# Performance work log

Hardware: AMD Instinct MI355X
Metric: run time of the kernel (lower is better)

The kernel has to match this reference:

```python
import jax, jax.numpy as jnp
import numpy as np

B, H, W, C = 2, 64, 64, 1024
L = H * W
HC, WC = 32, 32
NH, DH = 16, 64
NUM_REMAIN = 1638


def setup_inputs() -> dict:
    key = jax.random.key(0)
    ks = jax.random.split(key, 8)
    s = 1.0 / np.sqrt(C)
    x = jax.random.normal(ks[0], (B, L, C), jnp.float32)
    cached_x = jax.random.normal(ks[1], (B, HC, WC, C), jnp.float32)
    W_qkv = jax.random.normal(ks[2], (3 * C, C), jnp.float32) * s
    q_bias = jnp.zeros((C,), jnp.float32)
    v_bias = jnp.zeros((C,), jnp.float32)
    W_proj = jax.random.normal(ks[3], (C, C), jnp.float32) * s
    b_proj = jnp.zeros((C,), jnp.float32)
    scale_mul_log = jnp.full((1, NH, 1, 1), np.log(4.0), jnp.float32)
    # rope cache as (cos, sin) pairs over the flat token axis, DH//2 freqs
    ang = jax.random.uniform(ks[4], (L, DH // 2), jnp.float32) * (2 * np.pi)
    rope_grid = jnp.stack([jnp.cos(ang), jnp.sin(ang)], axis=0)  # (2, L, DH//2)
    return {"x": x, "cached_x": cached_x, "W_qkv": W_qkv, "q_bias": q_bias,
            "v_bias": v_bias, "W_proj": W_proj, "b_proj": b_proj,
            "scale_mul_log": scale_mul_log, "rope_grid": rope_grid,
            "num_remain": NUM_REMAIN}


def reference(x, cached_x, W_qkv, q_bias, v_bias, W_proj, b_proj,
              scale_mul_log, rope_grid, num_remain):
    Bx, Lx, Cx = x.shape
    # --- FastVAR token merge: MSE-to-spatial-mean selection (adaptive_avg_pool2d -> mean over L)
    mean_x = jnp.mean(x, axis=1, keepdims=True)                      # (B,1,C)
    mse = jnp.sum((x - mean_x) ** 2, axis=-1)                        # (B,L)
    idx = jnp.argsort(-mse, axis=1)[:, :num_remain]                  # (B,n) descending
    bix = jnp.arange(Bx)[:, None]
    xm = x[bix, idx]                                                 # (B,n,C) merged tokens
    # --- qkv projection with (q_bias, 0, v_bias)
    bias = jnp.concatenate([q_bias, jnp.zeros_like(q_bias), v_bias])
    qkv = (xm @ W_qkv.T + bias).reshape(Bx, -1, 3, NH, DH)
    qkv = qkv.transpose(2, 0, 3, 1, 4)                               # (3,B,H,n,dh)
    q, k, v = qkv[0], qkv[1], qkv[2]
    # --- cos attention: L2-normalize q,k; head-wise learned scale on q; sdpa scale = 1
    scale_mul = jnp.exp(jnp.minimum(scale_mul_log, jnp.log(100.0)))  # (1,NH,1,1)
    def l2n(t):
        return t / jnp.maximum(jnp.linalg.norm(t, axis=-1, keepdims=True), 1e-12)
    q = l2n(q) * scale_mul
    k = l2n(k)
    # --- 2D RoPE with per-sample gathered cache at the kept-token positions
    rc = rope_grid[:, idx, :]                                        # (2,B,n,DH//2)
    r0 = rc[0][:, None, :, :]                                        # (B,1,n,DH//2)
    r1 = rc[1][:, None, :, :]
    def rope(t):
        tp = t.reshape(*t.shape[:-1], DH // 2, 2)
        t0, t1 = tp[..., 0], tp[..., 1]
        return jnp.stack([r0 * t0 - r1 * t1, r1 * t0 + r0 * t1], axis=-1).reshape(t.shape)
    q = rope(q)
    k = rope(k)
    # --- attention over merged tokens
    attn = jax.nn.softmax(jnp.einsum('bhqd,bhkd->bhqk', q, k), axis=-1)
    o = jnp.einsum('bhqk,bhkd->bhqd', attn, v)                       # (B,H,n,dh)
    o = o.transpose(0, 2, 1, 3).reshape(Bx, -1, Cx)                  # (B,n,C)
    o = o @ W_proj.T + b_proj
    up = jnp.repeat(jnp.repeat(cached_x, 2, axis=1), 2, axis=2).reshape(Bx, Lx, Cx)
    out_full = up.at[bix, idx].set(o)
    return x + out_full
```

## Files before the change

### kernel.cpp

```cpp
#include <hip/hip_runtime.h>
#include <hip/hip_bf16.h>
#include <math.h>

#define BQ   2
#define LQ   4096
#define CQ   1024
#define NHQ  16
#define DHQ  64
#define KSEL 1638
#define KPAD 1664
#define MTOT (BQ*KSEL)
#define MPAD 3328

typedef short s16x8 __attribute__((ext_vector_type(8)));
typedef float fx4   __attribute__((ext_vector_type(4)));

#define MFMA16(a,b,c) __builtin_amdgcn_mfma_f32_16x16x32_bf16(a,b,c,0,0,0)

__device__ __forceinline__ float b2f(unsigned short u) {
  union { float f; unsigned int i; } cv; cv.i = ((unsigned int)u) << 16; return cv.f;
}
__device__ __forceinline__ unsigned short f2b(float f) {
  union { float f; unsigned int i; } cv; cv.f = f;
  unsigned int x = cv.i;
  return (unsigned short)((x + 0x7fffu + ((x >> 16) & 1u)) >> 16);
}
__device__ __forceinline__ unsigned int fbits(float f) {
  union { float f; unsigned int i; } cv; cv.f = f; return cv.i;
}
__device__ __forceinline__ unsigned int cvtpk_bf16(float a, float b) {
  unsigned int r;
  asm("v_cvt_pk_bf16_f32 %0, %1, %2" : "=v"(r) : "v"(a), "v"(b));
  return r;
}
__device__ __forceinline__ void async16(const void* g, void* l) {
  __builtin_amdgcn_global_load_lds((const __attribute__((address_space(1))) void*)g,
                                   (__attribute__((address_space(3))) void*)l, 16, 0, 0);
}
__device__ __forceinline__ float fexp2(float x) {
#if __has_builtin(__builtin_amdgcn_exp2f)
  return __builtin_amdgcn_exp2f(x);
#else
  return __expf(x * 0.69314718055994531f);
#endif
}

__global__ __launch_bounds__(256) void k_mean_part(const float* __restrict__ x,
                                                   double* __restrict__ part) {
  int bid = blockIdx.x;
  int cb = bid & 3, ch = (bid >> 2) & 31, b = bid >> 7;
  int c = cb * 256 + threadIdx.x;
  const float* p = x + ((size_t)b * LQ + (size_t)ch * 128) * CQ + c;
  double s = 0.0;
  for (int r = 0; r < 128; ++r) s += (double)p[(size_t)r * CQ];
  part[((size_t)b * 32 + ch) * CQ + c] = s;
}

__global__ __launch_bounds__(256) void k_mean_reduce(const double* __restrict__ part,
                                                     double* __restrict__ mean) {
  int g = blockIdx.x * 256 + threadIdx.x;
  int b = g >> 10, c = g & 1023;
  double s = 0.0;
  for (int ch = 0; ch < 32; ++ch) s += part[((size_t)b * 32 + ch) * CQ + c];
  mean[g] = s * (1.0 / 4096.0);
}

__global__ __launch_bounds__(256) void k_mse_base(const float* __restrict__ x,
                                                  const float* __restrict__ cached,
                                                  const double* __restrict__ mean,
                                                  double* __restrict__ mse,
                                                  float* __restrict__ out,
                                                  unsigned short* __restrict__ xb) {
  int bl = blockIdx.x; int b = bl >> 12, l = bl & 4095;
  int hh = l >> 6, ww = l & 63;
  size_t xoff = ((size_t)b * LQ + l) * CQ;
  size_t uoff = (((size_t)b * 32 + (hh >> 1)) * 32 + (ww >> 1)) * CQ;
  const double* mrow = mean + (size_t)b * CQ;
  int c0 = threadIdx.x * 4;
  float4 xv = *(const float4*)(x + xoff + c0);
  float4 uv = *(const float4*)(cached + uoff + c0);
  float4 ov;
  ov.x = xv.x + uv.x; ov.y = xv.y + uv.y; ov.z = xv.z + uv.z; ov.w = xv.w + uv.w;
  *(float4*)(out + xoff + c0) = ov;
  ushort4 xo;
  xo.x = f2b(xv.x); xo.y = f2b(xv.y); xo.z = f2b(xv.z); xo.w = f2b(xv.w);
  ((ushort4*)xb)[(xoff + c0) >> 2] = xo;
  double d0 = (double)xv.x - mrow[c0];
  double d1 = (double)xv.y - mrow[c0 + 1];
  double d2 = (double)xv.z - mrow[c0 + 2];
  double d3 = (double)xv.w - mrow[c0 + 3];
  double ss = d0 * d0 + d1 * d1 + d2 * d2 + d3 * d3;
  for (int o = 1; o < 64; o <<= 1) ss += __shfl_xor(ss, o);
  __shared__ double ws4[4];
  if ((threadIdx.x & 63) == 0) ws4[threadIdx.x >> 6] = ss;
  __syncthreads();
  if (threadIdx.x == 0) mse[(size_t)b * LQ + l] = ws4[0] + ws4[1] + ws4[2] + ws4[3];
}

__global__ __launch_bounds__(1024) void k_topk(const double* __restrict__ mse,
                                               int* __restrict__ idx_sel,
                                               const float* __restrict__ wqkv,
                                               const float* __restrict__ wproj,
                                               unsigned short* __restrict__ wqb,
                                               unsigned short* __restrict__ wpb) {
  if (blockIdx.x >= 2) {
    int i = (blockIdx.x - 2) * 1024 + threadIdx.x;
    const float* s; unsigned short* d; int off;
    if (i < 786432) { s = wqkv;  d = wqb; off = i; }
    else            { s = wproj; d = wpb; off = i - 786432; }
    float4 v = ((const float4*)s)[off];
    ushort4 o;
    o.x = f2b(v.x); o.y = f2b(v.y); o.z = f2b(v.z); o.w = f2b(v.w);
    ((ushort4*)d)[off] = o;
    return;
  }
  __shared__ unsigned long long u[4096];
  __shared__ unsigned int whist[16 * 257];
  __shared__ unsigned int wtot[4];
  __shared__ unsigned long long sh_prefix;
  __shared__ int sh_rem, sh_rem2, sh_bsel, sh_cnt, sh_eqcnt;
  __shared__ int eqbuf[256];
  int b = blockIdx.x, t = threadIdx.x;
  int wv = t >> 6, laneid = t & 63;
  for (int p = 0; p < 4; ++p) {
    int i = p * 1024 + t;
    u[i] = (unsigned long long)__double_as_longlong(mse[(size_t)b * LQ + i]);
  }
  if (t == 0) { sh_prefix = 0ULL; sh_rem = KSEL; sh_cnt = 0; sh_eqcnt = 0; }
  __syncthreads();
  for (int shift = 56; shift >= 0; shift -= 8) {
    for (int z = t; z < 16 * 257; z += 1024) whist[z] = 0u;
    __syncthreads();
    unsigned long long pref = sh_prefix;
#pragma unroll
    for (int p = 0; p < 4; ++p) {
      int i = p * 1024 + t;
      unsigned long long v = u[i];
      bool cand = (shift == 56) || ((v >> ((shift + 8) & 63)) == pref);
      if (cand) atomicAdd(&whist[wv * 257 + ((unsigned int)(v >> shift) & 255u)], 1u);
    }
    __syncthreads();
    unsigned int myc = 0, mysc = 0;
    if (t < 256) {
      unsigned int s = 0;
      int bin = 255 - t;
#pragma unroll
      for (int wvi = 0; wvi < 16; ++wvi) s += whist[wvi * 257 + bin];
      myc = s;
      mysc = myc;
#pragma unroll
      for (int o = 1; o < 64; o <<= 1) {
        unsigned int v2 = __shfl_up(mysc, o);
        if (laneid >= o) mysc += v2;
      }
      if (laneid == 63) wtot[wv] = mysc;
    }
    __syncthreads();
    if (t < 256) {
      unsigned int basep = 0;
      for (int wvi = 0; wvi < wv; ++wvi) basep += wtot[wvi];
      unsigned int incl = basep + mysc;
      unsigned int excl = incl - myc;
      unsigned int rem = (unsigned int)sh_rem;
      if (excl < rem && rem <= incl) {
        sh_bsel = 255 - t;
        sh_rem2 = (int)(rem - excl);
      }
    }
    __syncthreads();
    if (t == 0) {
      sh_prefix = (sh_prefix << 8) | (unsigned long long)sh_bsel;
      sh_rem = sh_rem2;
    }
    __syncthreads();
  }
  unsigned long long T = sh_prefix;
  int rem_eq = sh_rem;
#pragma unroll
  for (int p = 0; p < 4; ++p) {
    int i = p * 1024 + t;
    unsigned long long v = u[i];
    bool win = (v > T);
    unsigned long long mask = __ballot(win);
    int total = __popcll(mask);
    int base = 0;
    if (laneid == 0 && total > 0) base = atomicAdd(&sh_cnt, total);
    base = __shfl(base, 0);
    if (win) {
      int lpos = __popcll(mask & ((1ULL << laneid) - 1ULL));
      idx_sel[b * KPAD + base + lpos] = i;
    }
    if (v == T) {
      int e = atomicAdd(&sh_eqcnt, 1);
      if (e < 256) eqbuf[e] = i;
    }
  }
  __syncthreads();
  if (t == 0) {
    int n = sh_eqcnt; if (n > 256) n = 256;
    for (int a = 1; a < n; ++a) {
      int key = eqbuf[a]; int c = a - 1;
      while (c >= 0 && eqbuf[c] > key) { eqbuf[c + 1] = eqbuf[c]; --c; }
      eqbuf[c + 1] = key;
    }
    int base = sh_cnt;
    for (int a = 0; a < rem_eq && a < n; ++a) idx_sel[b * KPAD + base + a] = eqbuf[a];
    for (int a = KSEL; a < KPAD; ++a) idx_sel[b * KPAD + a] = 0;
  }
}

__global__ __launch_bounds__(256) void k_gemmA(const unsigned short* __restrict__ Asrc,
                                               const unsigned short* __restrict__ Bmat,
                                               const int* __restrict__ idx_sel,
                                               unsigned short* __restrict__ Cbf) {
  int bm = blockIdx.x % 26, bn = blockIdx.x / 26;
  int tid = threadIdx.x;
  int w = tid >> 6, lane = tid & 63, quad = lane >> 4, l15 = lane & 15;
  int wm = w & 1, wn = w >> 1;
  __shared__ __align__(16) unsigned char sm[3][16384];

  const unsigned short* gA[2];
  const unsigned short* gB[2];
#pragma unroll
  for (int p = 0; p < 2; ++p) {
    int e = p * 256 + tid; int row = e >> 2, kc = e & 3;
    int m = bm * 128 + row; if (m >= MTOT) m = MTOT - 1;
    int bb = m / KSEL; int ii = m - bb * KSEL;
    int lsel = idx_sel[bb * KPAD + ii];
    gA[p] = Asrc + ((size_t)bb * LQ + lsel) * CQ + kc * 8;
    gB[p] = Bmat + (size_t)(bn * 128 + row) * CQ + kc * 8;
  }

  fx4 acc[4][4];
#pragma unroll
  for (int a = 0; a < 4; ++a)
#pragma unroll
    for (int c = 0; c < 4; ++c) acc[a][c] = (fx4){0.f, 0.f, 0.f, 0.f};

#define STAGE_A(boff, it) do { int ke = (it) * 32;                                  \
    _Pragma("unroll")                                                               \
    for (int p = 0; p < 2; ++p) {                                                   \
      async16(gA[p] + ke, sm[0] + (boff) + p * 4096 + w * 1024);                    \
      async16(gB[p] + ke, sm[0] + (boff) + 8192 + p * 4096 + w * 1024);             \
    } } while (0)

  STAGE_A(0, 0);
  STAGE_A(16384, 1);
  for (int it = 0; it < 32; ++it) {
    int cur = it % 3;
    if (it + 2 < 32) STAGE_A(((it + 2) % 3) * 16384, it + 2);
    if (it <= 29)      asm volatile("s_waitcnt vmcnt(8)");
    else if (it == 30) asm volatile("s_waitcnt vmcnt(4)");
    else               asm volatile("s_waitcnt vmcnt(0)");
    __builtin_amdgcn_s_barrier();
    const unsigned char* smb = sm[0] + cur * 16384;
    s16x8 af[4], bf[4];
#pragma unroll
    for (int mt = 0; mt < 4; ++mt)
      af[mt] = *(const s16x8*)(smb + ((wm * 64 + mt * 16 + l15) * 64 + quad * 16));
#pragma unroll
    for (int nt = 0; nt < 4; ++nt)
      bf[nt] = *(const s16x8*)(smb + 8192 + ((wn * 64 + nt * 16 + l15) * 64 + quad * 16));
    __builtin_amdgcn_s_setprio(1);
#pragma unroll
    for (int mt = 0; mt < 4; ++mt)
#pragma unroll
      for (int nt = 0; nt < 4; ++nt)
        acc[mt][nt] = MFMA16(af[mt], bf[nt], acc[mt][nt]);
    __builtin_amdgcn_s_setprio(0);
    __builtin_amdgcn_s_barrier();
  }
#undef STAGE_A

#pragma unroll
  for (int mt = 0; mt < 4; ++mt)
#pragma unroll
    for (int nt = 0; nt < 4; ++nt) {
      int n = bn * 128 + wn * 64 + nt * 16 + l15;
      int mbase = bm * 128 + wm * 64 + mt * 16 + quad * 4;
      fx4 vv = acc[mt][nt];
#pragma unroll
      for (int r = 0; r < 4; ++r) {
        int m = mbase + r;
        if (m < MTOT) Cbf[(size_t)m * 3072 + n] = f2b(vv[r]);
      }
    }
}

__global__ __launch_bounds__(256) void k_gemmB(const unsigned short* __restrict__ Asrc,
                                               const unsigned short* __restrict__ Bmat,
                                               const int* __restrict__ idx_sel,
                                               float* __restrict__ Cf,
                                               const float* __restrict__ xin,
                                               const float* __restrict__ bproj) {
  int bid = blockIdx.x;
  int swz = (bid & 7) * 104 + (bid >> 3);
  int bm = swz % 52, bn = swz / 52;
  int tid = threadIdx.x;
  int w = tid >> 6, lane = tid & 63, quad = lane >> 4, l15 = lane & 15;
  int wm = w & 1, wn = w >> 1;
  __shared__ __align__(16) unsigned char sm[2][16384];

  const unsigned short* g4[4];
#pragma unroll
  for (int p = 0; p < 4; ++p) {
    int e = (p & 1) * 256 + tid; int row = e >> 3, kc = e & 7;
    if (p < 2) {
      int m = bm * 64 + row; if (m >= MTOT) m = MTOT - 1;
      int bb = m / KSEL; int ii = m - bb * KSEL;
      g4[p] = Asrc + ((size_t)bb * KPAD + ii) * CQ + kc * 8;
    } else {
      g4[p] = Bmat + (size_t)(bn * 64 + row) * CQ + kc * 8;
    }
  }

  fx4 acc[2][2];
#pragma unroll
  for (int a = 0; a < 2; ++a)
#pragma unroll
    for (int c = 0; c < 2; ++c) acc[a][c] = (fx4){0.f, 0.f, 0.f, 0.f};

#define STAGE_B(buf, it) do { int ke = (it) * 64;                                   \
    _Pragma("unroll")                                                               \
    for (int p = 0; p < 4; ++p)                                                     \
      async16(g4[p] + ke, sm[buf] + p * 4096 + w * 1024);                           \
    } while (0)

  STAGE_B(0, 0);
  for (int it = 0; it < 16; ++it) {
    int cur = it & 1;
    if (it < 15) STAGE_B(cur ^ 1, it + 1);
    if (it < 15) asm volatile("s_waitcnt vmcnt(4)");
    else         asm volatile("s_waitcnt vmcnt(0)");
    __builtin_amdgcn_s_barrier();
    const unsigned char* smb = sm[cur];
#pragma unroll
    for (int kk = 0; kk < 2; ++kk) {
      s16x8 af[2], bf2[2];
#pragma unroll
      for (int mt = 0; mt < 2; ++mt)
        af[mt] = *(const s16x8*)(smb + ((wm * 32 + mt * 16 + l15) * 64 + kk * 32 + quad * 8) * 2);
#pragma unroll
      for (int nt = 0; nt < 2; ++nt)
        bf2[nt] = *(const s16x8*)(smb + 8192 + ((wn * 32 + nt * 16 + l15) * 64 + kk * 32 + quad * 8) * 2);
#pragma unroll
      for (int mt = 0; mt < 2; ++mt)
#pragma unroll
        for (int nt = 0; nt < 2; ++nt)
          acc[mt][nt] = MFMA16(af[mt], bf2[nt], acc[mt][nt]);
    }
    __builtin_amdgcn_s_barrier();
  }
#undef STAGE_B

#pragma unroll
  for (int mt = 0; mt < 2; ++mt)
#pragma unroll
    for (int nt = 0; nt < 2; ++nt) {
      int n = bn * 64 + wn * 32 + nt * 16 + l15;
      int mbase = bm * 64 + wm * 32 + mt * 16 + quad * 4;
      fx4 vv = acc[mt][nt];
      float bp = bproj[n];
#pragma unroll
      for (int r = 0; r < 4; ++r) {
        int m = mbase + r;
        if (m < MTOT) {
          int bb = m / KSEL; int ii = m - bb * KSEL;
          int lsel = idx_sel[bb * KPAD + ii];
          size_t off = ((size_t)bb * LQ + lsel) * CQ + n;
          Cf[off] = xin[off] + vv[r] + bp;
        }
      }
    }
}

__global__ __launch_bounds__(256) void k_normrope(const unsigned short* __restrict__ qkv,
                                                  const int* __restrict__ idx_sel,
                                                  const float* __restrict__ qbias,
                                                  const float* __restrict__ vbias,
                                                  const float* __restrict__ sml,
                                                  const float* __restrict__ rope,
                                                  unsigned short* __restrict__ qo,
                                                  unsigned short* __restrict__ ko,
                                                  unsigned short* __restrict__ vt) {
  int bid = blockIdx.x;
  int tile = bid % 26; int h = (bid / 26) & 15; int b = bid / (26 * 16);
  int tid = threadIdx.x; int w = tid >> 6; int d = tid & 63;
  __shared__ unsigned short vtile[64 * 68];
  float scale = expf(fminf(sml[h], 4.6051702f)) * 1.4426950408889634f;
  float qb = qbias[h * 64 + d];
  float vb = vbias[h * 64 + d];
  for (int pass = 0; pass < 16; ++pass) {
    int il = pass * 4 + w;
    int i = tile * 64 + il;
    float vraw = 0.f;
    if (i < KSEL) {
      int lsel = idx_sel[b * KPAD + i];
      size_t base = ((size_t)(b * KSEL + i)) * 3072 + h * 64 + d;
      int tt = d >> 1;
      float r0 = rope[(size_t)lsel * 32 + tt];
      float r1 = rope[(size_t)LQ * 32 + (size_t)lsel * 32 + tt];
      float qv = b2f(qkv[base]) + qb;
      float ss = qv * qv;
      for (int o = 1; o < 64; o <<= 1) ss += __shfl_xor(ss, o);
      float qn = qv / fmaxf(sqrtf(ss), 1e-12f) * scale;
      float qp = __shfl_xor(qn, 1);
      float qr = (d & 1) ? (r1 * qp + r0 * qn) : (r0 * qn - r1 * qp);
      qo[((size_t)(b * NHQ + h) * KPAD + i) * 64 + d] = f2b(qr);
      float kv = b2f(qkv[base + 1024]);
      float ks = kv * kv;
      for (int o = 1; o < 64; o <<= 1) ks += __shfl_xor(ks, o);
      float kn = kv / fmaxf(sqrtf(ks), 1e-12f);
      float kp = __shfl_xor(kn, 1);
      float kr = (d & 1) ? (r1 * kp + r0 * kn) : (r0 * kn - r1 * kp);
      ko[((size_t)(b * NHQ + h) * KPAD + i) * 64 + d] = f2b(kr);
      vraw = b2f(qkv[base + 2048]) + vb;
    }
    vtile[d * 68 + il] = f2b(vraw);
  }
  __syncthreads();
  int row = tid >> 2, c0 = (tid & 3) * 16;
  s16x8 o0, o1;
#pragma unroll
  for (int jj = 0; jj < 8; ++jj) {
    o0[jj] = (short)vtile[row * 68 + c0 + jj];
    o1[jj] = (short)vtile[row * 68 + c0 + 8 + jj];
  }
  size_t doff = ((size_t)((b * NHQ + h) * 64 + row)) * KPAD + (size_t)tile * 64 + c0;
  *(s16x8*)(vt + doff) = o0;
  *(s16x8*)(vt + doff + 8) = o1;
}

__global__ __launch_bounds__(256, 4) void k_attn(const unsigned short* __restrict__ qb,
                                                 const unsigned short* __restrict__ kb,
                                                 const unsigned short* __restrict__ vtb,
                                                 const float* __restrict__ sml,
                                                 unsigned short* __restrict__ pO,
                                                 float* __restrict__ pl) {
  int qt = blockIdx.x; int bh = blockIdx.y; int part = blockIdx.z;
  int b = bh >> 4, h = bh & 15;
  int t0 = part * 13, t1 = t0 + 13;
  int q0 = qt * 128;
  int tid = threadIdx.x, w = tid >> 6, lane = tid & 63, quad = lane >> 4, l15 = lane & 15;
  float M = __expf(fminf(sml[h], 4.6051702f)) * 1.4426950408889634f;
  __shared__ __align__(16) unsigned short Kt[64 * 72];
  __shared__ __align__(16) unsigned short Vt[64 * 72];
  __shared__ __align__(16) unsigned short Pq[4][32 * 72];
  unsigned short* Pw = Pq[w];
  const unsigned short* qbase = qb + (size_t)(b * NHQ + h) * KPAD * 64;
  const unsigned short* kbase = kb + (size_t)(b * NHQ + h) * KPAD * 64;
  const unsigned short* vbase = vtb + (size_t)(b * NHQ + h) * 64 * KPAD;

  int r0 = tid >> 3, c0 = tid & 7;
  int r1 = 32 + r0, c1 = c0;

  s16x8 qf[2][2];
#pragma unroll
  for (int qtile = 0; qtile < 2; ++qtile)
#pragma unroll
    for (int kb2 = 0; kb2 < 2; ++kb2) {
      int row = q0 + w * 32 + qtile * 16 + l15;
      qf[qtile][kb2] = *(const s16x8*)(qbase + (size_t)row * 64 + kb2 * 32 + quad * 8);
    }

  float lsum[2] = {0.f, 0.f};
  fx4 oacc[2][4];
#pragma unroll
  for (int qtile = 0; qtile < 2; ++qtile)
#pragma unroll
    for (int dt = 0; dt < 4; ++dt) oacc[qtile][dt] = (fx4){0.f, 0.f, 0.f, 0.f};

  s16x8 kn0, kn1, vn0, vn1;
  {
    int j0 = t0 * 64;
    kn0 = *(const s16x8*)(kbase + (size_t)(j0 + r0) * 64 + c0 * 8);
    kn1 = *(const s16x8*)(kbase + (size_t)(j0 + r1) * 64 + c1 * 8);
    vn0 = *(const s16x8*)(vbase + (size_t)r0 * KPAD + j0 + c0 * 8);
    vn1 = *(const s16x8*)(vbase + (size_t)r1 * KPAD + j0 + c1 * 8);
  }

  for (int t = t0; t < t1; ++t) {
    int j0 = t * 64;
    bool tail = (j0 + 64 > KSEL);
    __builtin_amdgcn_s_barrier();
    *(s16x8*)(Kt + r0 * 72 + c0 * 8) = kn0;
    *(s16x8*)(Kt + r1 * 72 + c1 * 8) = kn1;
    *(s16x8*)(Vt + r0 * 72 + c0 * 8) = vn0;
    *(s16x8*)(Vt + r1 * 72 + c1 * 8) = vn1;
    if (t + 1 < t1) {
      int jn = (t + 1) * 64;
      kn0 = *(const s16x8*)(kbase + (size_t)(jn + r0) * 64 + c0 * 8);
      kn1 = *(const s16x8*)(kbase + (size_t)(jn + r1) * 64 + c1 * 8);
      vn0 = *(const s16x8*)(vbase + (size_t)r0 * KPAD + jn + c0 * 8);
      vn1 = *(const s16x8*)(vbase + (size_t)r1 * KPAD + jn + c1 * 8);
    }
    asm volatile("s_waitcnt lgkmcnt(0)" ::: "memory");
    __builtin_amdgcn_s_barrier();

    fx4 sacc[2][4];
#pragma unroll
    for (int qtile = 0; qtile < 2; ++qtile)
#pragma unroll
      for (int jj = 0; jj < 4; ++jj) sacc[qtile][jj] = (fx4){0.f, 0.f, 0.f, 0.f};
    __builtin_amdgcn_s_setprio(1);
#pragma unroll
    for (int jj = 0; jj < 4; ++jj) {
      int jl = jj * 16 + l15;
      s16x8 kf0 = *(const s16x8*)(Kt + jl * 72 + quad * 8);
      s16x8 kf1 = *(const s16x8*)(Kt + jl * 72 + 32 + quad * 8);
      sacc[0][jj] = MFMA16(kf0, qf[0][0], sacc[0][jj]);
      sacc[1][jj] = MFMA16(kf0, qf[1][0], sacc[1][jj]);
      sacc[0][jj] = MFMA16(kf1, qf[0][1], sacc[0][jj]);
      sacc[1][jj] = MFMA16(kf1, qf[1][1], sacc[1][jj]);
    }
    __builtin_amdgcn_s_setprio(0);
#pragma unroll
    for (int qtile = 0; qtile < 2; ++qtile)
#pragma unroll
      for (int jj = 0; jj < 4; ++jj) {
        int jbase = j0 + jj * 16 + quad * 4;
        fx4 sv = sacc[qtile][jj];
        float p0 = fexp2(sv[0] - M);
        float p1 = fexp2(sv[1] - M);
        float p2 = fexp2(sv[2] - M);
        float p3 = fexp2(sv[3] - M);
        if (tail) {
          if (jbase + 0 >= KSEL) p0 = 0.f;
          if (jbase + 1 >= KSEL) p1 = 0.f;
          if (jbase + 2 >= KSEL) p2 = 0.f;
          if (jbase + 3 >= KSEL) p3 = 0.f;
        }
        lsum[qtile] += (p0 + p1) + (p2 + p3);
        *(uint2*)(Pw + (qtile * 16 + l15) * 72 + jj * 16 + quad * 4) =
            make_uint2(cvtpk_bf16(p0, p1), cvtpk_bf16(p2, p3));
      }
    __builtin_amdgcn_s_setprio(1);
#pragma unroll
    for (int js = 0; js < 2; ++js) {
      s16x8 pf0 = *(const s16x8*)(Pw + l15 * 72 + js * 32 + quad * 8);
      s16x8 pf1 = *(const s16x8*)(Pw + (16 + l15) * 72 + js * 32 + quad * 8);
#pragma unroll
      for (int dt = 0; dt < 4; ++dt) {
        s16x8 vf = *(const s16x8*)(Vt + (dt * 16 + l15) * 72 + js * 32 + quad * 8);
        oacc[0][dt] = MFMA16(pf0, vf, oacc[0][dt]);
        oacc[1][dt] = MFMA16(pf1, vf, oacc[1][dt]);
      }
    }
    __builtin_amdgcn_s_setprio(0);
  }

#pragma unroll
  for (int qtile = 0; qtile < 2; ++qtile) {
    float s = lsum[qtile];
    s += __shfl_xor(s, 16);
    s += __shfl_xor(s, 32);
    lsum[qtile] = s;
  }

  size_t pbase = (((size_t)part * 2 + b) * NHQ + h) * KPAD;
#pragma unroll
  for (int qtile = 0; qtile < 2; ++qtile) {
    int gqb = q0 + w * 32 + qtile * 16;
    if (quad == 0) pl[pbase + gqb + l15] = lsum[qtile];
  }

#pragma unroll
  for (int qtile = 0; qtile < 2; ++qtile)
#pragma unroll
    for (int dt = 0; dt < 4; ++dt)
#pragma unroll
      for (int r = 0; r < 4; ++r)
        Pw[(qtile * 16 + quad * 4 + r) * 72 + dt * 16 + l15] = f2b(oacc[qtile][dt][r]);
#pragma unroll
  for (int pass = 0; pass < 4; ++pass) {
    int row = pass * 8 + (lane >> 3), chunk = lane & 7;
    s16x8 vv = *(const s16x8*)(Pw + row * 72 + chunk * 8);
    *(s16x8*)(pO + (pbase + q0 + w * 32 + row) * 64 + chunk * 8) = vv;
  }
}

__global__ __launch_bounds__(256) void k_comb(const unsigned short* __restrict__ pO,
                                              const float* __restrict__ pl,
                                              unsigned short* __restrict__ ob) {
  size_t g = (size_t)blockIdx.x * 256 + threadIdx.x;
  int d = (int)(g & 63);
  size_t row = g >> 6;
  int gq = (int)(row % KPAD);
  int bhh = (int)(row / KPAD);
  int b = bhh >> 4, h = bhh & 15;
  float oa = b2f(pO[g]);
  float obv = b2f(pO[g + 3407872]);
  float la = pl[row], lb = pl[row + 53248];
  float o = (oa + obv) / (la + lb);
  ob[((size_t)(b * KPAD + gq)) * CQ + h * 64 + d] = f2b(o);
}

extern "C" void kernel_launch(void* const* d_in, const int* in_sizes, int n_in,
                              void* d_out, int out_size, void* d_ws, size_t ws_size,
                              hipStream_t stream) {
  const float* x      = (const float*)d_in[0];
  const float* cached = (const float*)d_in[1];
  const float* wqkv   = (const float*)d_in[2];
  const float* qbias  = (const float*)d_in[3];
  const float* vbias  = (const float*)d_in[4];
  const float* wproj  = (const float*)d_in[5];
  const float* bproj  = (const float*)d_in[6];
  const float* sml    = (const float*)d_in[7];
  const float* rope   = (const float*)d_in[8];
  float* out = (float*)d_out;
  char* ws = (char*)d_ws;

  double* meanpart        = (double*)(ws);
  double* mean            = (double*)(ws + 524288);
  double* mse             = (double*)(ws + 540672);
  int* idx_sel            = (int*)(ws + 606208);
  unsigned short* x_bf    = (unsigned short*)(ws + 619520);
  unsigned short* wqkv_bf = (unsigned short*)(ws + 17396736);
  unsigned short* qkv     = (unsigned short*)(ws + 23688192);
  unsigned short* pO      = (unsigned short*)(ws + 619520);
  float* pl               = (float*)(ws + 14251008);
  unsigned short* wproj_bf= (unsigned short*)(ws + 44135424);
  unsigned short* qo      = (unsigned short*)(ws + 46232576);
  unsigned short* ko      = (unsigned short*)(ws + 53048320);
  unsigned short* vt      = (unsigned short*)(ws + 59864064);
  unsigned short* ob      = (unsigned short*)(ws + 66679808);

  hipLaunchKernelGGL(k_mean_part, dim3(256), dim3(256), 0, stream, x, meanpart);
  hipLaunchKernelGGL(k_mean_reduce, dim3(8), dim3(256), 0, stream, meanpart, mean);
  hipLaunchKernelGGL(k_mse_base, dim3(8192), dim3(256), 0, stream, x, cached, mean, mse,
                     out, x_bf);
  hipLaunchKernelGGL(k_topk, dim3(2 + 1024), dim3(1024), 0, stream, mse, idx_sel,
                     wqkv, wproj, wqkv_bf, wproj_bf);
  hipLaunchKernelGGL(k_gemmA, dim3(26 * 24), dim3(256), 0, stream,
                     x_bf, wqkv_bf, idx_sel, qkv);
  hipLaunchKernelGGL(k_normrope, dim3(26 * 16 * BQ), dim3(256), 0, stream,
                     qkv, idx_sel, qbias, vbias, sml, rope, qo, ko, vt);
  hipLaunchKernelGGL(k_attn, dim3(13, BQ * NHQ, 2), dim3(256), 0, stream,
                     qo, ko, vt, sml, pO, pl);
  hipLaunchKernelGGL(k_comb, dim3(13312), dim3(256), 0, stream, pO, pl, ob);
  hipLaunchKernelGGL(k_gemmB, dim3(832), dim3(256), 0, stream,
                     ob, wproj_bf, idx_sel, out, x, bproj);
}
```

Before: 282.7 us.

## Split attention KV range four ways and shrink P buffer for occupancy

Attention now splits the key range into four partitions (7,7,6,6 tiles) instead of two, doubling the block count. To raise occupancy (launch bounds 8), the per-warp P staging buffer is halved: softmax and the PV MFMAs are interleaved per 32-key half, and the output epilogue is written in two halves. The combine kernel sums four partials and the partial-sum buffer is moved to make room. The cost is more partial-output traffic and a heavier combine step.

```diff
diff --git a/kernel.cpp b/kernel.cpp
--- a/kernel.cpp
+++ b/kernel.cpp
@@ -431,7 +431,7 @@
   *(s16x8*)(vt + doff + 8) = o1;
 }
 
-__global__ __launch_bounds__(256, 4) void k_attn(const unsigned short* __restrict__ qb,
+__global__ __launch_bounds__(256, 8) void k_attn(const unsigned short* __restrict__ qb,
                                                  const unsigned short* __restrict__ kb,
                                                  const unsigned short* __restrict__ vtb,
                                                  const float* __restrict__ sml,
@@ -439,13 +439,15 @@
                                                  float* __restrict__ pl) {
   int qt = blockIdx.x; int bh = blockIdx.y; int part = blockIdx.z;
   int b = bh >> 4, h = bh & 15;
-  int t0 = part * 13, t1 = t0 + 13;
+  int t0, t1;
+  if (part < 2) { t0 = part * 7; t1 = t0 + 7; }
+  else          { t0 = 14 + (part - 2) * 6; t1 = t0 + 6; }
   int q0 = qt * 128;
   int tid = threadIdx.x, w = tid >> 6, lane = tid & 63, quad = lane >> 4, l15 = lane & 15;
   float M = __expf(fminf(sml[h], 4.6051702f)) * 1.4426950408889634f;
   __shared__ __align__(16) unsigned short Kt[64 * 72];
   __shared__ __align__(16) unsigned short Vt[64 * 72];
-  __shared__ __align__(16) unsigned short Pq[4][32 * 72];
+  __shared__ __align__(16) unsigned short Pq[4][32 * 40];
   unsigned short* Pw = Pq[w];
   const unsigned short* qbase = qb + (size_t)(b * NHQ + h) * KPAD * 64;
   const unsigned short* kbase = kb + (size_t)(b * NHQ + h) * KPAD * 64;
@@ -514,39 +516,43 @@
       sacc[1][jj] = MFMA16(kf1, qf[1][1], sacc[1][jj]);
     }
     __builtin_amdgcn_s_setprio(0);
-#pragma unroll
-    for (int qtile = 0; qtile < 2; ++qtile)
-#pragma unroll
-      for (int jj = 0; jj < 4; ++jj) {
-        int jbase = j0 + jj * 16 + quad * 4;
-        fx4 sv = sacc[qtile][jj];
-        float p0 = fexp2(sv[0] - M);
-        float p1 = fexp2(sv[1] - M);
-        float p2 = fexp2(sv[2] - M);
-        float p3 = fexp2(sv[3] - M);
-        if (tail) {
-          if (jbase + 0 >= KSEL) p0 = 0.f;
-          if (jbase + 1 >= KSEL) p1 = 0.f;
-          if (jbase + 2 >= KSEL) p2 = 0.f;
-          if (jbase + 3 >= KSEL) p3 = 0.f;
+
+#pragma unroll
+    for (int js = 0; js < 2; ++js) {
+#pragma unroll
+      for (int qtile = 0; qtile < 2; ++qtile)
+#pragma unroll
+        for (int jg = 0; jg < 2; ++jg) {
+          int jj = js * 2 + jg;
+          int jbase = j0 + jj * 16 + quad * 4;
+          fx4 sv = sacc[qtile][jj];
+          float p0 = fexp2(sv[0] - M);
+          float p1 = fexp2(sv[1] - M);
+          float p2 = fexp2(sv[2] - M);
+          float p3 = fexp2(sv[3] - M);
+          if (tail) {
+            if (jbase + 0 >= KSEL) p0 = 0.f;
+            if (jbase + 1 >= KSEL) p1 = 0.f;
+            if (jbase + 2 >= KSEL) p2 = 0.f;
+            if (jbase + 3 >= KSEL) p3 = 0.f;
+          }
+          lsum[qtile] += (p0 + p1) + (p2 + p3);
+          *(uint2*)(Pw + (qtile * 16 + l15) * 40 + jg * 16 + quad * 4) =
+              make_uint2(cvtpk_bf16(p0, p1), cvtpk_bf16(p2, p3));
         }
-        lsum[qtile] += (p0 + p1) + (p2 + p3);
-        *(uint2*)(Pw + (qtile * 16 + l15) * 72 + jj * 16 + quad * 4) =
-            make_uint2(cvtpk_bf16(p0, p1), cvtpk_bf16(p2, p3));
+      __builtin_amdgcn_s_setprio(1);
+      {
+        s16x8 pf0 = *(const s16x8*)(Pw + l15 * 40 + quad * 8);
+        s16x8 pf1 = *(const s16x8*)(Pw + (16 + l15) * 40 + quad * 8);
+#pragma unroll
+        for (int dt = 0; dt < 4; ++dt) {
+          s16x8 vf = *(const s16x8*)(Vt + (dt * 16 + l15) * 72 + js * 32 + quad * 8);
+          oacc[0][dt] = MFMA16(pf0, vf, oacc[0][dt]);
+          oacc[1][dt] = MFMA16(pf1, vf, oacc[1][dt]);
+        }
       }
-    __builtin_amdgcn_s_setprio(1);
-#pragma unroll
-    for (int js = 0; js < 2; ++js) {
-      s16x8 pf0 = *(const s16x8*)(Pw + l15 * 72 + js * 32 + quad * 8);
-      s16x8 pf1 = *(const s16x8*)(Pw + (16 + l15) * 72 + js * 32 + quad * 8);
-#pragma unroll
-      for (int dt = 0; dt < 4; ++dt) {
-        s16x8 vf = *(const s16x8*)(Vt + (dt * 16 + l15) * 72 + js * 32 + quad * 8);
-        oacc[0][dt] = MFMA16(pf0, vf, oacc[0][dt]);
-        oacc[1][dt] = MFMA16(pf1, vf, oacc[1][dt]);
-      }
-    }
-    __builtin_amdgcn_s_setprio(0);
+      __builtin_amdgcn_s_setprio(0);
+    }
   }
 
 #pragma unroll
@@ -565,17 +571,23 @@
   }
 
 #pragma unroll
-  for (int qtile = 0; qtile < 2; ++qtile)
-#pragma unroll
-    for (int dt = 0; dt < 4; ++dt)
-#pragma unroll
-      for (int r = 0; r < 4; ++r)
-        Pw[(qtile * 16 + quad * 4 + r) * 72 + dt * 16 + l15] = f2b(oacc[qtile][dt][r]);
-#pragma unroll
-  for (int pass = 0; pass < 4; ++pass) {
-    int row = pass * 8 + (lane >> 3), chunk = lane & 7;
-    s16x8 vv = *(const s16x8*)(Pw + row * 72 + chunk * 8);
-    *(s16x8*)(pO + (pbase + q0 + w * 32 + row) * 64 + chunk * 8) = vv;
+  for (int half = 0; half < 2; ++half) {
+    __builtin_amdgcn_s_barrier();
+#pragma unroll
+    for (int qtile = 0; qtile < 2; ++qtile)
+#pragma unroll
+      for (int dt = 0; dt < 2; ++dt)
+#pragma unroll
+        for (int r = 0; r < 4; ++r)
+          Pw[(qtile * 16 + quad * 4 + r) * 40 + dt * 16 + l15] =
+              f2b(oacc[qtile][half * 2 + dt][r]);
+    asm volatile("s_waitcnt lgkmcnt(0)" ::: "memory");
+#pragma unroll
+    for (int pass = 0; pass < 2; ++pass) {
+      int row = pass * 16 + (lane >> 2), chunk = lane & 3;
+      s16x8 vv = *(const s16x8*)(Pw + row * 40 + chunk * 8);
+      *(s16x8*)(pO + (pbase + q0 + w * 32 + row) * 64 + half * 32 + chunk * 8) = vv;
+    }
   }
 }
 
@@ -588,10 +600,13 @@
   int gq = (int)(row % KPAD);
   int bhh = (int)(row / KPAD);
   int b = bhh >> 4, h = bhh & 15;
-  float oa = b2f(pO[g]);
-  float obv = b2f(pO[g + 3407872]);
-  float la = pl[row], lb = pl[row + 53248];
-  float o = (oa + obv) / (la + lb);
+  float osum = 0.f, lsumv = 0.f;
+#pragma unroll
+  for (int p = 0; p < 4; ++p) {
+    osum += b2f(pO[g + (size_t)p * 3407872]);
+    lsumv += pl[row + (size_t)p * 53248];
+  }
+  float o = osum / lsumv;
   ob[((size_t)(b * KPAD + gq)) * CQ + h * 64 + d] = f2b(o);
 }
 
@@ -618,7 +633,7 @@
   unsigned short* wqkv_bf = (unsigned short*)(ws + 17396736);
   unsigned short* qkv     = (unsigned short*)(ws + 23688192);
   unsigned short* pO      = (unsigned short*)(ws + 619520);
-  float* pl               = (float*)(ws + 14251008);
+  float* pl               = (float*)(ws + 27882496);
   unsigned short* wproj_bf= (unsigned short*)(ws + 44135424);
   unsigned short* qo      = (unsigned short*)(ws + 46232576);
   unsigned short* ko      = (unsigned short*)(ws + 53048320);
@@ -635,7 +650,7 @@
                      x_bf, wqkv_bf, idx_sel, qkv);
   hipLaunchKernelGGL(k_normrope, dim3(26 * 16 * BQ), dim3(256), 0, stream,
                      qkv, idx_sel, qbias, vbias, sml, rope, qo, ko, vt);
-  hipLaunchKernelGGL(k_attn, dim3(13, BQ * NHQ, 2), dim3(256), 0, stream,
+  hipLaunchKernelGGL(k_attn, dim3(13, BQ * NHQ, 4), dim3(256), 0, stream,
                      qo, ko, vt, sml, pO, pl);
   hipLaunchKernelGGL(k_comb, dim3(13312), dim3(256), 0, stream, pO, pl, ob);
   hipLaunchKernelGGL(k_gemmB, dim3(832), dim3(256), 0, stream,
```

New measurement: 290.4 us. 2.7% more time.

## Shrink QKV GEMM tile to 64x128 with double buffering; vectorize norm-rope

Applied to the files above, without the earlier changes.

The QKV projection GEMM now uses 64-row M tiles instead of 128 and a two-stage LDS buffer instead of three. That doubles the grid to 1248 blocks so more CUs have work, and it reduces LDS and accumulator use per block. The cost is less data reuse per tile and a shallower prefetch pipeline. Separately, the norm+RoPE kernel now has each lane handle a pair of dims with 32-bit loads and stores, two tokens per wave, and shorter shuffle reductions.

```diff
diff --git a/kernel.cpp b/kernel.cpp
--- a/kernel.cpp
+++ b/kernel.cpp
@@ -213,57 +213,56 @@
                                                const unsigned short* __restrict__ Bmat,
                                                const int* __restrict__ idx_sel,
                                                unsigned short* __restrict__ Cbf) {
-  int bm = blockIdx.x % 26, bn = blockIdx.x / 26;
+  int bm = blockIdx.x % 52, bn = blockIdx.x / 52;
   int tid = threadIdx.x;
   int w = tid >> 6, lane = tid & 63, quad = lane >> 4, l15 = lane & 15;
   int wm = w & 1, wn = w >> 1;
-  __shared__ __align__(16) unsigned char sm[3][16384];
-
-  const unsigned short* gA[2];
+  __shared__ __align__(16) unsigned char sm[2][12288];
+
+  const unsigned short* gA;
+  {
+    int row = tid >> 2, kc = tid & 3;
+    int m = bm * 64 + row; if (m >= MTOT) m = MTOT - 1;
+    int bb = m / KSEL; int ii = m - bb * KSEL;
+    int lsel = idx_sel[bb * KPAD + ii];
+    gA = Asrc + ((size_t)bb * LQ + lsel) * CQ + kc * 8;
+  }
   const unsigned short* gB[2];
 #pragma unroll
   for (int p = 0; p < 2; ++p) {
     int e = p * 256 + tid; int row = e >> 2, kc = e & 3;
-    int m = bm * 128 + row; if (m >= MTOT) m = MTOT - 1;
-    int bb = m / KSEL; int ii = m - bb * KSEL;
-    int lsel = idx_sel[bb * KPAD + ii];
-    gA[p] = Asrc + ((size_t)bb * LQ + lsel) * CQ + kc * 8;
     gB[p] = Bmat + (size_t)(bn * 128 + row) * CQ + kc * 8;
   }
 
-  fx4 acc[4][4];
-#pragma unroll
-  for (int a = 0; a < 4; ++a)
+  fx4 acc[2][4];
+#pragma unroll
+  for (int a = 0; a < 2; ++a)
 #pragma unroll
     for (int c = 0; c < 4; ++c) acc[a][c] = (fx4){0.f, 0.f, 0.f, 0.f};
 
-#define STAGE_A(boff, it) do { int ke = (it) * 32;                                  \
-    _Pragma("unroll")                                                               \
-    for (int p = 0; p < 2; ++p) {                                                   \
-      async16(gA[p] + ke, sm[0] + (boff) + p * 4096 + w * 1024);                    \
-      async16(gB[p] + ke, sm[0] + (boff) + 8192 + p * 4096 + w * 1024);             \
-    } } while (0)
+#define STAGE_A(buf, it) do { int ke = (it) * 32;                                   \
+    async16(gA + ke, sm[buf] + tid * 16);                                           \
+    async16(gB[0] + ke, sm[buf] + 4096 + tid * 16);                                 \
+    async16(gB[1] + ke, sm[buf] + 8192 + tid * 16); } while (0)
 
   STAGE_A(0, 0);
-  STAGE_A(16384, 1);
   for (int it = 0; it < 32; ++it) {
-    int cur = it % 3;
-    if (it + 2 < 32) STAGE_A(((it + 2) % 3) * 16384, it + 2);
-    if (it <= 29)      asm volatile("s_waitcnt vmcnt(8)");
-    else if (it == 30) asm volatile("s_waitcnt vmcnt(4)");
-    else               asm volatile("s_waitcnt vmcnt(0)");
+    int cur = it & 1;
+    if (it < 31) STAGE_A(cur ^ 1, it + 1);
+    if (it < 31) asm volatile("s_waitcnt vmcnt(3)");
+    else         asm volatile("s_waitcnt vmcnt(0)");
     __builtin_amdgcn_s_barrier();
-    const unsigned char* smb = sm[0] + cur * 16384;
-    s16x8 af[4], bf[4];
-#pragma unroll
-    for (int mt = 0; mt < 4; ++mt)
-      af[mt] = *(const s16x8*)(smb + ((wm * 64 + mt * 16 + l15) * 64 + quad * 16));
+    const unsigned char* smb = sm[cur];
+    s16x8 af[2], bf[4];
+#pragma unroll
+    for (int mt = 0; mt < 2; ++mt)
+      af[mt] = *(const s16x8*)(smb + ((wm * 32 + mt * 16 + l15) * 32 + quad * 8) * 2);
 #pragma unroll
     for (int nt = 0; nt < 4; ++nt)
-      bf[nt] = *(const s16x8*)(smb + 8192 + ((wn * 64 + nt * 16 + l15) * 64 + quad * 16));
+      bf[nt] = *(const s16x8*)(smb + 4096 + ((wn * 64 + nt * 16 + l15) * 32 + quad * 8) * 2);
     __builtin_amdgcn_s_setprio(1);
 #pragma unroll
-    for (int mt = 0; mt < 4; ++mt)
+    for (int mt = 0; mt < 2; ++mt)
 #pragma unroll
       for (int nt = 0; nt < 4; ++nt)
         acc[mt][nt] = MFMA16(af[mt], bf[nt], acc[mt][nt]);
@@ -273,11 +272,11 @@
 #undef STAGE_A
 
 #pragma unroll
-  for (int mt = 0; mt < 4; ++mt)
+  for (int mt = 0; mt < 2; ++mt)
 #pragma unroll
     for (int nt = 0; nt < 4; ++nt) {
       int n = bn * 128 + wn * 64 + nt * 16 + l15;
-      int mbase = bm * 128 + wm * 64 + mt * 16 + quad * 4;
+      int mbase = bm * 64 + wm * 32 + mt * 16 + quad * 4;
       fx4 vv = acc[mt][nt];
 #pragma unroll
       for (int r = 0; r < 4; ++r) {
@@ -385,38 +384,48 @@
                                                   unsigned short* __restrict__ vt) {
   int bid = blockIdx.x;
   int tile = bid % 26; int h = (bid / 26) & 15; int b = bid / (26 * 16);
-  int tid = threadIdx.x; int w = tid >> 6; int d = tid & 63;
+  int tid = threadIdx.x; int w = tid >> 6; int lane = tid & 63;
+  int tk = lane >> 5, dl = lane & 31;
+  int d0 = dl * 2;
   __shared__ unsigned short vtile[64 * 68];
   float scale = expf(fminf(sml[h], 4.6051702f)) * 1.4426950408889634f;
-  float qb = qbias[h * 64 + d];
-  float vb = vbias[h * 64 + d];
-  for (int pass = 0; pass < 16; ++pass) {
-    int il = pass * 4 + w;
+  float2 qb2 = *(const float2*)(qbias + h * 64 + d0);
+  float2 vb2 = *(const float2*)(vbias + h * 64 + d0);
+  for (int pass = 0; pass < 8; ++pass) {
+    int il = pass * 8 + w * 2 + tk;
     int i = tile * 64 + il;
-    float vraw = 0.f;
+    float v0 = 0.f, v1 = 0.f;
     if (i < KSEL) {
       int lsel = idx_sel[b * KPAD + i];
-      size_t base = ((size_t)(b * KSEL + i)) * 3072 + h * 64 + d;
-      int tt = d >> 1;
-      float r0 = rope[(size_t)lsel * 32 + tt];
-      float r1 = rope[(size_t)LQ * 32 + (size_t)lsel * 32 + tt];
-      float qv = b2f(qkv[base]) + qb;
-      float ss = qv * qv;
-      for (int o = 1; o < 64; o <<= 1) ss += __shfl_xor(ss, o);
-      float qn = qv / fmaxf(sqrtf(ss), 1e-12f) * scale;
-      float qp = __shfl_xor(qn, 1);
-      float qr = (d & 1) ? (r1 * qp + r0 * qn) : (r0 * qn - r1 * qp);
-      qo[((size_t)(b * NHQ + h) * KPAD + i) * 64 + d] = f2b(qr);
-      float kv = b2f(qkv[base + 1024]);
-      float ks = kv * kv;
-      for (int o = 1; o < 64; o <<= 1) ks += __shfl_xor(ks, o);
-      float kn = kv / fmaxf(sqrtf(ks), 1e-12f);
-      float kp = __shfl_xor(kn, 1);
-      float kr = (d & 1) ? (r1 * kp + r0 * kn) : (r0 * kn - r1 * kp);
-      ko[((size_t)(b * NHQ + h) * KPAD + i) * 64 + d] = f2b(kr);
-      vraw = b2f(qkv[base + 2048]) + vb;
-    }
-    vtile[d * 68 + il] = f2b(vraw);
+      size_t base = ((size_t)(b * KSEL + i)) * 3072 + h * 64 + d0;
+      float r0 = rope[(size_t)lsel * 32 + dl];
+      float r1 = rope[(size_t)LQ * 32 + (size_t)lsel * 32 + dl];
+      unsigned int qw = *(const unsigned int*)(qkv + base);
+      float q0 = b2f((unsigned short)qw) + qb2.x;
+      float q1 = b2f((unsigned short)(qw >> 16)) + qb2.y;
+      float ss = q0 * q0 + q1 * q1;
+#pragma unroll
+      for (int o = 1; o < 32; o <<= 1) ss += __shfl_xor(ss, o);
+      float rn = scale / fmaxf(sqrtf(ss), 1e-12f);
+      float qn0 = q0 * rn, qn1 = q1 * rn;
+      *(unsigned int*)(qo + ((size_t)(b * NHQ + h) * KPAD + i) * 64 + d0) =
+          cvtpk_bf16(r0 * qn0 - r1 * qn1, r1 * qn0 + r0 * qn1);
+      unsigned int kw = *(const unsigned int*)(qkv + base + 1024);
+      float k0 = b2f((unsigned short)kw);
+      float k1 = b2f((unsigned short)(kw >> 16));
+      float ks = k0 * k0 + k1 * k1;
+#pragma unroll
+      for (int o = 1; o < 32; o <<= 1) ks += __shfl_xor(ks, o);
+      float rkn = 1.0f / fmaxf(sqrtf(ks), 1e-12f);
+      float kn0 = k0 * rkn, kn1 = k1 * rkn;
+      *(unsigned int*)(ko + ((size_t)(b * NHQ + h) * KPAD + i) * 64 + d0) =
+          cvtpk_bf16(r0 * kn0 - r1 * kn1, r1 * kn0 + r0 * kn1);
+      unsigned int vw = *(const unsigned int*)(qkv + base + 2048);
+      v0 = b2f((unsigned short)vw) + vb2.x;
+      v1 = b2f((unsigned short)(vw >> 16)) + vb2.y;
+    }
+    vtile[d0 * 68 + il] = f2b(v0);
+    vtile[(d0 + 1) * 68 + il] = f2b(v1);
   }
   __syncthreads();
   int row = tid >> 2, c0 = (tid & 3) * 16;
@@ -631,7 +640,7 @@
                      out, x_bf);
   hipLaunchKernelGGL(k_topk, dim3(2 + 1024), dim3(1024), 0, stream, mse, idx_sel,
                      wqkv, wproj, wqkv_bf, wproj_bf);
-  hipLaunchKernelGGL(k_gemmA, dim3(26 * 24), dim3(256), 0, stream,
+  hipLaunchKernelGGL(k_gemmA, dim3(52 * 24), dim3(256), 0, stream,
                      x_bf, wqkv_bf, idx_sel, qkv);
   hipLaunchKernelGGL(k_normrope, dim3(26 * 16 * BQ), dim3(256), 0, stream,
                      qkv, idx_sel, qbias, vbias, sml, rope, qo, ko, vt);
```

New measurement: 279.5 us. No clear change (-1.1%).
